# Performance work log

Hardware: AMD Instinct MI355X
Metric: run time of the kernel (lower is better)

## Reference

```python
import jax, jax.numpy as jnp
import numpy as np


def _interp_linear_align_corners(w, new_len):
    """Linear (bilinear with trivial 2nd axis) interpolation along last axis,
    align_corners=True, matching torch F.interpolate. w: (..., k) -> (..., new_len)."""
    k = w.shape[-1]
    scale = (k - 1) / (new_len - 1) if new_len > 1 else 0.0
    pos = jnp.arange(new_len, dtype=w.dtype) * jnp.asarray(scale, w.dtype)
    lo = jnp.floor(pos).astype(jnp.int32)
    hi = jnp.minimum(lo + 1, k - 1)
    frac = pos - lo.astype(w.dtype)
    return w[..., lo] * (1.0 - frac) + w[..., hi] * frac


def _depthwise_conv(x, kernel, pad_h, pad_w):
    # x: (B,C,H,W), kernel: (C,1,Kh,Kw), groups=C
    C = x.shape[1]
    return jax.lax.conv_general_dilated(
        x, kernel, window_strides=(1, 1),
        padding=[(pad_h, pad_h), (pad_w, pad_w)],
        dimension_numbers=("NCHW", "OIHW", "NCHW"),
        feature_group_count=C)


def setup_inputs() -> dict:
    key = jax.random.key(0)
    k1, k2, k3, k4, k5 = jax.random.split(key, 5)
    dim, ksize = 128, 13
    B, H, W = 32, 64, 64
    fan = 1.0 / np.sqrt(ksize)  # torch Conv2d default init scale (groups=dim -> fan_in=k)
    return {
        "x": jax.random.normal(k1, (B, dim, H, W), dtype=jnp.float32),
        "h_weight": jax.random.uniform(k2, (dim, 1, ksize, 1), jnp.float32, -fan, fan),
        "w_weight": jax.random.uniform(k3, (dim, 1, 1, ksize), jnp.float32, -fan, fan),
        "h_bias": jax.random.uniform(k4, (dim,), jnp.float32, -fan, fan),
        "w_bias": jax.random.uniform(k5, (dim,), jnp.float32, -fan, fan),
    }


def reference(x, h_weight, w_weight, h_bias, w_bias):
    B, C, H, W = x.shape
    Kh, Kw = 2 * H - 1, 2 * W - 1
    # Interpolate base kernels to instance kernel sizes (align_corners=True bilinear,
    # degenerate to 1-D linear since the other spatial dim has size 1).
    hk = _interp_linear_align_corners(h_weight[:, :, :, 0], Kh)[..., None]   # (C,1,Kh,1)
    wk = _interp_linear_align_corners(w_weight[:, :, 0, :], Kw)[:, :, None]  # (C,1,1,Kw)
    y = _depthwise_conv(x, hk, H - 1, 0) + h_bias[None, :, None, None]
    y = _depthwise_conv(y, wk, 0, W - 1) + w_bias[None, :, None, None]
    return y
```

## Files before the change

kernel.cpp:

```cpp
#include <hip/hip_runtime.h>


#define STRB 72

typedef short  bfrag  __attribute__((ext_vector_type(8)));
typedef float  f32x4  __attribute__((ext_vector_type(4)));
typedef unsigned short us4 __attribute__((ext_vector_type(4)));

__device__ __forceinline__ unsigned short f2bf(float f) {
    unsigned u = __builtin_bit_cast(unsigned, f);
    u += 0x7fffu + ((u >> 16) & 1u);
    return (unsigned short)(u >> 16);
}

__device__ __forceinline__ void lds_barrier() {
    asm volatile("s_waitcnt lgkmcnt(0)" ::: "memory");
    __builtin_amdgcn_s_barrier();
}

__global__ __launch_bounds__(256, 4)
void oversize_conv_mfma4(const float* __restrict__ x,
                         const float* __restrict__ hwt,
                         const float* __restrict__ wwt,
                         const float* __restrict__ hb,
                         const float* __restrict__ wb,
                         float* __restrict__ out)
{
    __shared__ __align__(16) unsigned short Xs[64 * STRB];
    __shared__ __align__(16) unsigned short Aw[64 * STRB];
    __shared__ __align__(16) unsigned short Ah[64 * STRB];
    __shared__ __align__(16) unsigned short PT[64 * STRB];
    __shared__ float hk[128], wk[128], sw[64];

    const int tid = threadIdx.x;
    const int c   = blockIdx.x & 127;
    const int g4  = blockIdx.x >> 7;
    const size_t img0      = ((size_t)(4 * g4) * 128 + c) * 4096;
    const size_t imgStride = (size_t)128 * 4096;

    const int wv = tid >> 6, lane = tid & 63;
    const int r = lane & 15, gq = lane >> 4;

    float4 xv[4];
    {
        const float4* xg = (const float4*)(x + img0);
        #pragma unroll
        for (int i = 0; i < 4; ++i) xv[i] = xg[tid + i * 256];
    }

    if (tid < 127) {
        const float scale = 12.0f / 126.0f;
        float pos = (float)tid * scale;
        int   lo  = (int)pos;
        float fr  = pos - (float)lo;
        int   hi  = (lo + 1 < 12) ? lo + 1 : 12;
        hk[tid] = hwt[c * 13 + lo] * (1.0f - fr) + hwt[c * 13 + hi] * fr;
        wk[tid] = wwt[c * 13 + lo] * (1.0f - fr) + wwt[c * 13 + hi] * fr;
    }
    lds_barrier();

    {
        const int row = tid >> 2;
        const int cb  = (tid & 3) * 16;
        #pragma unroll
        for (int q = 0; q < 4; ++q) {
            us4 vh, vw;
            #pragma unroll
            for (int j = 0; j < 4; ++j) {
                int col = cb + q * 4 + j;
                vh[j] = f2bf(hk[col - row + 63]);
                vw[j] = f2bf(wk[col - row + 63]);
            }
            *(us4*)&Ah[row * STRB + cb + q * 4] = vh;
            *(us4*)&Aw[row * STRB + cb + q * 4] = vw;
        }
    }
    if (tid < 64) {
        float s = 0.f;
        #pragma unroll 8
        for (int iw = 0; iw < 64; ++iw) s += wk[iw - tid + 63];
        sw[tid] = s;
    }
    #pragma unroll
    for (int i = 0; i < 4; ++i) {
        int idx = tid + i * 256;
        int row = idx >> 4;
        int col = (idx & 15) * 4;
        us4 v;
        v[0] = f2bf(xv[i].x); v[1] = f2bf(xv[i].y);
        v[2] = f2bf(xv[i].z); v[3] = f2bf(xv[i].w);
        *(us4*)&Xs[row * STRB + col] = v;
    }
    lds_barrier();

    const float hbc = hb[c], wbc = wb[c];
    float bias_nt[4];
    #pragma unroll
    for (int nt = 0; nt < 4; ++nt) bias_nt[nt] = hbc * sw[nt * 16 + r] + wbc;

    float4 xn[4];

    #pragma unroll
    for (int i = 0; i < 4; ++i) {
        if (i < 3) {
            const float4* xg = (const float4*)(x + img0 + (size_t)(i + 1) * imgStride);
            #pragma unroll
            for (int q = 0; q < 4; ++q) xn[q] = xg[tid + q * 256];
        }

        f32x4 acc[4] = {};
        {
            bfrag a0 = *(const bfrag*)&Xs[(wv * 16 + r) * STRB + gq * 8];
            bfrag a1 = *(const bfrag*)&Xs[(wv * 16 + r) * STRB + 32 + gq * 8];
            #pragma unroll
            for (int nt = 0; nt < 4; ++nt) {
                bfrag b0 = *(const bfrag*)&Aw[(nt * 16 + r) * STRB + gq * 8];
                bfrag b1 = *(const bfrag*)&Aw[(nt * 16 + r) * STRB + 32 + gq * 8];
                acc[nt] = __builtin_amdgcn_mfma_f32_16x16x32_bf16(a0, b0, acc[nt], 0, 0, 0);
                acc[nt] = __builtin_amdgcn_mfma_f32_16x16x32_bf16(a1, b1, acc[nt], 0, 0, 0);
            }
        }
        #pragma unroll
        for (int nt = 0; nt < 4; ++nt) {
            us4 p;
            p[0] = f2bf(acc[nt][0]); p[1] = f2bf(acc[nt][1]);
            p[2] = f2bf(acc[nt][2]); p[3] = f2bf(acc[nt][3]);
            *(us4*)&PT[(nt * 16 + r) * STRB + wv * 16 + gq * 4] = p;
        }
        lds_barrier();

        f32x4 acc2[4];
        #pragma unroll
        for (int nt = 0; nt < 4; ++nt) {
            float bv = bias_nt[nt];
            acc2[nt] = (f32x4){bv, bv, bv, bv};
        }
        {
            bfrag a0 = *(const bfrag*)&Ah[(wv * 16 + r) * STRB + gq * 8];
            bfrag a1 = *(const bfrag*)&Ah[(wv * 16 + r) * STRB + 32 + gq * 8];
            #pragma unroll
            for (int nt = 0; nt < 4; ++nt) {
                bfrag b0 = *(const bfrag*)&PT[(nt * 16 + r) * STRB + gq * 8];
                bfrag b1 = *(const bfrag*)&PT[(nt * 16 + r) * STRB + 32 + gq * 8];
                acc2[nt] = __builtin_amdgcn_mfma_f32_16x16x32_bf16(a0, b0, acc2[nt], 0, 0, 0);
                acc2[nt] = __builtin_amdgcn_mfma_f32_16x16x32_bf16(a1, b1, acc2[nt], 0, 0, 0);
            }
        }

        if (i < 3) {
            #pragma unroll
            for (int q = 0; q < 4; ++q) {
                int idx = tid + q * 256;
                int row = idx >> 4;
                int col = (idx & 15) * 4;
                us4 v;
                v[0] = f2bf(xn[q].x); v[1] = f2bf(xn[q].y);
                v[2] = f2bf(xn[q].z); v[3] = f2bf(xn[q].w);
                *(us4*)&Xs[row * STRB + col] = v;
            }
        }

        {
            float* og = out + img0 + (size_t)i * imgStride;
            #pragma unroll
            for (int nt = 0; nt < 4; ++nt) {
                #pragma unroll
                for (int j = 0; j < 4; ++j)
                    og[(size_t)(wv * 16 + gq * 4 + j) * 64 + nt * 16 + r] = acc2[nt][j];
            }
        }

        lds_barrier();
    }
}

extern "C" void kernel_launch(void* const* d_in, const int* in_sizes, int n_in,
                              void* d_out, int out_size, void* d_ws, size_t ws_size,
                              hipStream_t stream)
{
    const float* x   = (const float*)d_in[0];
    const float* hwt = (const float*)d_in[1];
    const float* wwt = (const float*)d_in[2];
    const float* hb  = (const float*)d_in[3];
    const float* wb  = (const float*)d_in[4];
    oversize_conv_mfma4<<<1024, 256, 0, stream>>>(x, hwt, wwt, hb, wb, (float*)d_out);
}
```

Before: 25.99 us.

## Load X fragments directly to registers, halve images per block, vectorize stores

X tiles are now read straight from global memory into MFMA A-fragments, so the Xs LDS staging buffer and its extra barrier pass go away. Each block now handles 2 images instead of 4, doubling the grid to 2048 blocks and raising launch bounds occupancy to 5. The second GEMM swaps operands so the PT tile is the A fragment and the output can be written as float4 stores along contiguous rows. The column-sum for the bias is split across all threads with a partial reduction. Smaller per-block work means the Toeplitz matrices are rebuilt more often, and the uncoalesced fragment-shaped global loads could cost bandwidth.

Measured after the change: 27.36 us. 1.05x slower.

```diff
diff --git a/kernel.cpp b/kernel.cpp
--- a/kernel.cpp
+++ b/kernel.cpp
@@ -18,35 +18,34 @@
     __builtin_amdgcn_s_barrier();
 }
 
-__global__ __launch_bounds__(256, 4)
-void oversize_conv_mfma4(const float* __restrict__ x,
+__global__ __launch_bounds__(256, 5)
+void oversize_conv_mfma2(const float* __restrict__ x,
                          const float* __restrict__ hwt,
                          const float* __restrict__ wwt,
                          const float* __restrict__ hb,
                          const float* __restrict__ wb,
                          float* __restrict__ out)
 {
-    __shared__ __align__(16) unsigned short Xs[64 * STRB];
     __shared__ __align__(16) unsigned short Aw[64 * STRB];
     __shared__ __align__(16) unsigned short Ah[64 * STRB];
     __shared__ __align__(16) unsigned short PT[64 * STRB];
-    __shared__ float hk[128], wk[128], sw[64];
+    __shared__ float hk[128], wk[128], swp[256];
+    __shared__ __align__(16) float sw[64];
 
     const int tid = threadIdx.x;
     const int c   = blockIdx.x & 127;
-    const int g4  = blockIdx.x >> 7;
-    const size_t img0      = ((size_t)(4 * g4) * 128 + c) * 4096;
+    const int bb  = (blockIdx.x >> 7) * 2;
+    const size_t img0      = ((size_t)bb * 128 + c) * 4096;
     const size_t imgStride = (size_t)128 * 4096;
 
     const int wv = tid >> 6, lane = tid & 63;
     const int r = lane & 15, gq = lane >> 4;
 
-    float4 xv[4];
-    {
-        const float4* xg = (const float4*)(x + img0);
-        #pragma unroll
-        for (int i = 0; i < 4; ++i) xv[i] = xg[tid + i * 256];
-    }
+    const float4* xrow0 = (const float4*)(x + img0 + (size_t)(16 * wv + r) * 64);
+    float4 xa0 = xrow0[2 * gq];
+    float4 xa1 = xrow0[2 * gq + 1];
+    float4 xa2 = xrow0[8 + 2 * gq];
+    float4 xa3 = xrow0[9 + 2 * gq];
 
     if (tid < 127) {
         const float scale = 12.0f / 126.0f;
@@ -75,50 +74,46 @@
             *(us4*)&Aw[row * STRB + cb + q * 4] = vw;
         }
     }
-    if (tid < 64) {
+    {
+        const int ow = tid >> 2, q = tid & 3;
         float s = 0.f;
-        #pragma unroll 8
-        for (int iw = 0; iw < 64; ++iw) s += wk[iw - tid + 63];
-        sw[tid] = s;
-    }
-    #pragma unroll
-    for (int i = 0; i < 4; ++i) {
-        int idx = tid + i * 256;
-        int row = idx >> 4;
-        int col = (idx & 15) * 4;
-        us4 v;
-        v[0] = f2bf(xv[i].x); v[1] = f2bf(xv[i].y);
-        v[2] = f2bf(xv[i].z); v[3] = f2bf(xv[i].w);
-        *(us4*)&Xs[row * STRB + col] = v;
+        #pragma unroll
+        for (int i = 0; i < 16; ++i) s += wk[(q * 16 + i) - ow + 63];
+        swp[tid] = s;
     }
     lds_barrier();
+    if (tid < 64)
+        sw[tid] = swp[4 * tid] + swp[4 * tid + 1] + swp[4 * tid + 2] + swp[4 * tid + 3];
 
     const float hbc = hb[c], wbc = wb[c];
-    float bias_nt[4];
-    #pragma unroll
-    for (int nt = 0; nt < 4; ++nt) bias_nt[nt] = hbc * sw[nt * 16 + r] + wbc;
-
-    float4 xn[4];
 
     #pragma unroll
-    for (int i = 0; i < 4; ++i) {
-        if (i < 3) {
-            const float4* xg = (const float4*)(x + img0 + (size_t)(i + 1) * imgStride);
-            #pragma unroll
-            for (int q = 0; q < 4; ++q) xn[q] = xg[tid + q * 256];
+    for (int i = 0; i < 2; ++i) {
+        bfrag a0, a1;
+        a0[0] = (short)f2bf(xa0.x); a0[1] = (short)f2bf(xa0.y);
+        a0[2] = (short)f2bf(xa0.z); a0[3] = (short)f2bf(xa0.w);
+        a0[4] = (short)f2bf(xa1.x); a0[5] = (short)f2bf(xa1.y);
+        a0[6] = (short)f2bf(xa1.z); a0[7] = (short)f2bf(xa1.w);
+        a1[0] = (short)f2bf(xa2.x); a1[1] = (short)f2bf(xa2.y);
+        a1[2] = (short)f2bf(xa2.z); a1[3] = (short)f2bf(xa2.w);
+        a1[4] = (short)f2bf(xa3.x); a1[5] = (short)f2bf(xa3.y);
+        a1[6] = (short)f2bf(xa3.z); a1[7] = (short)f2bf(xa3.w);
+
+        if (i == 0) {
+            const float4* xr = (const float4*)(x + img0 + imgStride + (size_t)(16 * wv + r) * 64);
+            xa0 = xr[2 * gq];
+            xa1 = xr[2 * gq + 1];
+            xa2 = xr[8 + 2 * gq];
+            xa3 = xr[9 + 2 * gq];
         }
 
         f32x4 acc[4] = {};
-        {
-            bfrag a0 = *(const bfrag*)&Xs[(wv * 16 + r) * STRB + gq * 8];
-            bfrag a1 = *(const bfrag*)&Xs[(wv * 16 + r) * STRB + 32 + gq * 8];
-            #pragma unroll
-            for (int nt = 0; nt < 4; ++nt) {
-                bfrag b0 = *(const bfrag*)&Aw[(nt * 16 + r) * STRB + gq * 8];
-                bfrag b1 = *(const bfrag*)&Aw[(nt * 16 + r) * STRB + 32 + gq * 8];
-                acc[nt] = __builtin_amdgcn_mfma_f32_16x16x32_bf16(a0, b0, acc[nt], 0, 0, 0);
-                acc[nt] = __builtin_amdgcn_mfma_f32_16x16x32_bf16(a1, b1, acc[nt], 0, 0, 0);
-            }
+        #pragma unroll
+        for (int nt = 0; nt < 4; ++nt) {
+            bfrag b0 = *(const bfrag*)&Aw[(nt * 16 + r) * STRB + gq * 8];
+            bfrag b1 = *(const bfrag*)&Aw[(nt * 16 + r) * STRB + 32 + gq * 8];
+            acc[nt] = __builtin_amdgcn_mfma_f32_16x16x32_bf16(a0, b0, acc[nt], 0, 0, 0);
+            acc[nt] = __builtin_amdgcn_mfma_f32_16x16x32_bf16(a1, b1, acc[nt], 0, 0, 0);
         }
         #pragma unroll
         for (int nt = 0; nt < 4; ++nt) {
@@ -129,45 +124,29 @@
         }
         lds_barrier();
 
-        f32x4 acc2[4];
+        f32x4 sw4 = *(const f32x4*)&sw[16 * wv + 4 * gq];
+        f32x4 bias;
+        bias[0] = hbc * sw4[0] + wbc; bias[1] = hbc * sw4[1] + wbc;
+        bias[2] = hbc * sw4[2] + wbc; bias[3] = hbc * sw4[3] + wbc;
+
+        bfrag pa0 = *(const bfrag*)&PT[(16 * wv + r) * STRB + gq * 8];
+        bfrag pa1 = *(const bfrag*)&PT[(16 * wv + r) * STRB + 32 + gq * 8];
+        f32x4 acc2[4] = {bias, bias, bias, bias};
         #pragma unroll
         for (int nt = 0; nt < 4; ++nt) {
-            float bv = bias_nt[nt];
-            acc2[nt] = (f32x4){bv, bv, bv, bv};
-        }
-        {
-            bfrag a0 = *(const bfrag*)&Ah[(wv * 16 + r) * STRB + gq * 8];
-            bfrag a1 = *(const bfrag*)&Ah[(wv * 16 + r) * STRB + 32 + gq * 8];
-            #pragma unroll
-            for (int nt = 0; nt < 4; ++nt) {
-                bfrag b0 = *(const bfrag*)&PT[(nt * 16 + r) * STRB + gq * 8];
-                bfrag b1 = *(const bfrag*)&PT[(nt * 16 + r) * STRB + 32 + gq * 8];
-                acc2[nt] = __builtin_amdgcn_mfma_f32_16x16x32_bf16(a0, b0, acc2[nt], 0, 0, 0);
-                acc2[nt] = __builtin_amdgcn_mfma_f32_16x16x32_bf16(a1, b1, acc2[nt], 0, 0, 0);
-            }
+            bfrag bh0 = *(const bfrag*)&Ah[(nt * 16 + r) * STRB + gq * 8];
+            bfrag bh1 = *(const bfrag*)&Ah[(nt * 16 + r) * STRB + 32 + gq * 8];
+            acc2[nt] = __builtin_amdgcn_mfma_f32_16x16x32_bf16(pa0, bh0, acc2[nt], 0, 0, 0);
+            acc2[nt] = __builtin_amdgcn_mfma_f32_16x16x32_bf16(pa1, bh1, acc2[nt], 0, 0, 0);
         }
 
-        if (i < 3) {
-            #pragma unroll
-            for (int q = 0; q < 4; ++q) {
-                int idx = tid + q * 256;
-                int row = idx >> 4;
-                int col = (idx & 15) * 4;
-                us4 v;
-                v[0] = f2bf(xn[q].x); v[1] = f2bf(xn[q].y);
-                v[2] = f2bf(xn[q].z); v[3] = f2bf(xn[q].w);
-                *(us4*)&Xs[row * STRB + col] = v;
-            }
-        }
-
-        {
-            float* og = out + img0 + (size_t)i * imgStride;
-            #pragma unroll
-            for (int nt = 0; nt < 4; ++nt) {
-                #pragma unroll
-                for (int j = 0; j < 4; ++j)
-                    og[(size_t)(wv * 16 + gq * 4 + j) * 64 + nt * 16 + r] = acc2[nt][j];
-            }
+        float* og = out + img0 + (size_t)i * imgStride;
+        #pragma unroll
+        for (int nt = 0; nt < 4; ++nt) {
+            float4 v;
+            v.x = acc2[nt][0]; v.y = acc2[nt][1];
+            v.z = acc2[nt][2]; v.w = acc2[nt][3];
+            *(float4*)&og[(size_t)(nt * 16 + r) * 64 + 16 * wv + 4 * gq] = v;
         }
 
         lds_barrier();
@@ -183,5 +162,5 @@
     const float* wwt = (const float*)d_in[2];
     const float* hb  = (const float*)d_in[3];
     const float* wb  = (const float*)d_in[4];
-    oversize_conv_mfma4<<<1024, 256, 0, stream>>>(x, hwt, wwt, hb, wb, (float*)d_out);
+    oversize_conv_mfma2<<<2048, 256, 0, stream>>>(x, hwt, wwt, hb, wb, (float*)d_out);
 }
```

## Swap second GEMM operands for vectorized nontemporal stores and earlier prefetch

Applied to the files above, without the earlier changes.

The second MFMA stage now takes the intermediate tile PT as the A operand and the height kernel as B. The output fragment becomes row-contiguous, so each lane writes a float4 with a nontemporal store instead of four strided scalar stores. The next image's global load is issued before the first barrier and overlapped with the following iteration's compute. The bias row-sum reduction is also split across all 256 threads instead of 64. The intended gain is wider, fully coalesced output writes and more latency hiding, in exchange for a changed bias layout and higher register pressure from the longer-lived prefetch.

Measured after the change: 30.43 us. 17.1% more time.

```diff
diff --git a/kernel.cpp b/kernel.cpp
--- a/kernel.cpp
+++ b/kernel.cpp
@@ -19,24 +19,25 @@
 }
 
 __global__ __launch_bounds__(256, 4)
-void oversize_conv_mfma4(const float* __restrict__ x,
-                         const float* __restrict__ hwt,
-                         const float* __restrict__ wwt,
-                         const float* __restrict__ hb,
-                         const float* __restrict__ wb,
-                         float* __restrict__ out)
+void oversize_conv_v5(const float* __restrict__ x,
+                      const float* __restrict__ hwt,
+                      const float* __restrict__ wwt,
+                      const float* __restrict__ hb,
+                      const float* __restrict__ wb,
+                      float* __restrict__ out)
 {
     __shared__ __align__(16) unsigned short Xs[64 * STRB];
     __shared__ __align__(16) unsigned short Aw[64 * STRB];
     __shared__ __align__(16) unsigned short Ah[64 * STRB];
     __shared__ __align__(16) unsigned short PT[64 * STRB];
-    __shared__ float hk[128], wk[128], sw[64];
+    __shared__ float hk[128], wk[128], swp[256];
+    __shared__ __align__(16) float sw[64];
 
     const int tid = threadIdx.x;
     const int c   = blockIdx.x & 127;
     const int g4  = blockIdx.x >> 7;
-    const size_t img0      = ((size_t)(4 * g4) * 128 + c) * 4096;
     const size_t imgStride = (size_t)128 * 4096;
+    const size_t img0 = ((size_t)(4 * g4) * 128 + c) * 4096;
 
     const int wv = tid >> 6, lane = tid & 63;
     const int r = lane & 15, gq = lane >> 4;
@@ -45,7 +46,7 @@
     {
         const float4* xg = (const float4*)(x + img0);
         #pragma unroll
-        for (int i = 0; i < 4; ++i) xv[i] = xg[tid + i * 256];
+        for (int q = 0; q < 4; ++q) xv[q] = xg[tid + q * 256];
     }
 
     if (tid < 127) {
@@ -75,76 +76,71 @@
             *(us4*)&Aw[row * STRB + cb + q * 4] = vw;
         }
     }
-    if (tid < 64) {
+    {
+        const int ow = tid >> 2, q = tid & 3;
         float s = 0.f;
-        #pragma unroll 8
-        for (int iw = 0; iw < 64; ++iw) s += wk[iw - tid + 63];
-        sw[tid] = s;
+        #pragma unroll
+        for (int i = 0; i < 16; ++i) s += wk[(q * 16 + i) - ow + 63];
+        swp[tid] = s;
     }
     #pragma unroll
-    for (int i = 0; i < 4; ++i) {
-        int idx = tid + i * 256;
+    for (int q = 0; q < 4; ++q) {
+        int idx = tid + q * 256;
         int row = idx >> 4;
         int col = (idx & 15) * 4;
         us4 v;
-        v[0] = f2bf(xv[i].x); v[1] = f2bf(xv[i].y);
-        v[2] = f2bf(xv[i].z); v[3] = f2bf(xv[i].w);
+        v[0] = f2bf(xv[q].x); v[1] = f2bf(xv[q].y);
+        v[2] = f2bf(xv[q].z); v[3] = f2bf(xv[q].w);
         *(us4*)&Xs[row * STRB + col] = v;
+    }
+    float4 xn[4];
+    {
+        const float4* xg = (const float4*)(x + img0 + imgStride);
+        #pragma unroll
+        for (int q = 0; q < 4; ++q) xn[q] = xg[tid + q * 256];
     }
     lds_barrier();
 
+    if (tid < 64)
+        sw[tid] = swp[4 * tid] + swp[4 * tid + 1] + swp[4 * tid + 2] + swp[4 * tid + 3];
+
     const float hbc = hb[c], wbc = wb[c];
-    float bias_nt[4];
-    #pragma unroll
-    for (int nt = 0; nt < 4; ++nt) bias_nt[nt] = hbc * sw[nt * 16 + r] + wbc;
-
-    float4 xn[4];
 
     #pragma unroll
     for (int i = 0; i < 4; ++i) {
-        if (i < 3) {
-            const float4* xg = (const float4*)(x + img0 + (size_t)(i + 1) * imgStride);
-            #pragma unroll
-            for (int q = 0; q < 4; ++q) xn[q] = xg[tid + q * 256];
-        }
-
+        bfrag a0 = *(const bfrag*)&Xs[(16 * wv + r) * STRB + 8 * gq];
+        bfrag a1 = *(const bfrag*)&Xs[(16 * wv + r) * STRB + 32 + 8 * gq];
         f32x4 acc[4] = {};
-        {
-            bfrag a0 = *(const bfrag*)&Xs[(wv * 16 + r) * STRB + gq * 8];
-            bfrag a1 = *(const bfrag*)&Xs[(wv * 16 + r) * STRB + 32 + gq * 8];
-            #pragma unroll
-            for (int nt = 0; nt < 4; ++nt) {
-                bfrag b0 = *(const bfrag*)&Aw[(nt * 16 + r) * STRB + gq * 8];
-                bfrag b1 = *(const bfrag*)&Aw[(nt * 16 + r) * STRB + 32 + gq * 8];
-                acc[nt] = __builtin_amdgcn_mfma_f32_16x16x32_bf16(a0, b0, acc[nt], 0, 0, 0);
-                acc[nt] = __builtin_amdgcn_mfma_f32_16x16x32_bf16(a1, b1, acc[nt], 0, 0, 0);
-            }
+        #pragma unroll
+        for (int nt = 0; nt < 4; ++nt) {
+            bfrag b0 = *(const bfrag*)&Aw[(16 * nt + r) * STRB + 8 * gq];
+            bfrag b1 = *(const bfrag*)&Aw[(16 * nt + r) * STRB + 32 + 8 * gq];
+            acc[nt] = __builtin_amdgcn_mfma_f32_16x16x32_bf16(a0, b0, acc[nt], 0, 0, 0);
+            acc[nt] = __builtin_amdgcn_mfma_f32_16x16x32_bf16(a1, b1, acc[nt], 0, 0, 0);
         }
         #pragma unroll
         for (int nt = 0; nt < 4; ++nt) {
             us4 p;
             p[0] = f2bf(acc[nt][0]); p[1] = f2bf(acc[nt][1]);
             p[2] = f2bf(acc[nt][2]); p[3] = f2bf(acc[nt][3]);
-            *(us4*)&PT[(nt * 16 + r) * STRB + wv * 16 + gq * 4] = p;
+            *(us4*)&PT[(16 * nt + r) * STRB + 16 * wv + 4 * gq] = p;
         }
         lds_barrier();
 
-        f32x4 acc2[4];
+        f32x4 sw4 = *(const f32x4*)&sw[16 * wv + 4 * gq];
+        f32x4 bias;
+        bias[0] = hbc * sw4[0] + wbc; bias[1] = hbc * sw4[1] + wbc;
+        bias[2] = hbc * sw4[2] + wbc; bias[3] = hbc * sw4[3] + wbc;
+
+        bfrag pa0 = *(const bfrag*)&PT[(16 * wv + r) * STRB + 8 * gq];
+        bfrag pa1 = *(const bfrag*)&PT[(16 * wv + r) * STRB + 32 + 8 * gq];
+        f32x4 acc2[4] = {bias, bias, bias, bias};
         #pragma unroll
         for (int nt = 0; nt < 4; ++nt) {
-            float bv = bias_nt[nt];
-            acc2[nt] = (f32x4){bv, bv, bv, bv};
-        }
-        {
-            bfrag a0 = *(const bfrag*)&Ah[(wv * 16 + r) * STRB + gq * 8];
-            bfrag a1 = *(const bfrag*)&Ah[(wv * 16 + r) * STRB + 32 + gq * 8];
-            #pragma unroll
-            for (int nt = 0; nt < 4; ++nt) {
-                bfrag b0 = *(const bfrag*)&PT[(nt * 16 + r) * STRB + gq * 8];
-                bfrag b1 = *(const bfrag*)&PT[(nt * 16 + r) * STRB + 32 + gq * 8];
-                acc2[nt] = __builtin_amdgcn_mfma_f32_16x16x32_bf16(a0, b0, acc2[nt], 0, 0, 0);
-                acc2[nt] = __builtin_amdgcn_mfma_f32_16x16x32_bf16(a1, b1, acc2[nt], 0, 0, 0);
-            }
+            bfrag bh0 = *(const bfrag*)&Ah[(16 * nt + r) * STRB + 8 * gq];
+            bfrag bh1 = *(const bfrag*)&Ah[(16 * nt + r) * STRB + 32 + 8 * gq];
+            acc2[nt] = __builtin_amdgcn_mfma_f32_16x16x32_bf16(pa0, bh0, acc2[nt], 0, 0, 0);
+            acc2[nt] = __builtin_amdgcn_mfma_f32_16x16x32_bf16(pa1, bh1, acc2[nt], 0, 0, 0);
         }
 
         if (i < 3) {
@@ -159,14 +155,19 @@
                 *(us4*)&Xs[row * STRB + col] = v;
             }
         }
+        if (i < 2) {
+            const float4* xg = (const float4*)(x + img0 + (size_t)(i + 2) * imgStride);
+            #pragma unroll
+            for (int q = 0; q < 4; ++q) xn[q] = xg[tid + q * 256];
+        }
 
         {
             float* og = out + img0 + (size_t)i * imgStride;
             #pragma unroll
             for (int nt = 0; nt < 4; ++nt) {
-                #pragma unroll
-                for (int j = 0; j < 4; ++j)
-                    og[(size_t)(wv * 16 + gq * 4 + j) * 64 + nt * 16 + r] = acc2[nt][j];
+                __builtin_nontemporal_store(
+                    acc2[nt],
+                    (f32x4*)&og[(size_t)(16 * nt + r) * 64 + 16 * wv + 4 * gq]);
             }
         }
 
@@ -183,5 +184,5 @@
     const float* wwt = (const float*)d_in[2];
     const float* hb  = (const float*)d_in[3];
     const float* wb  = (const float*)d_in[4];
-    oversize_conv_mfma4<<<1024, 256, 0, stream>>>(x, hwt, wwt, hb, wb, (float*)d_out);
+    oversize_conv_v5<<<1024, 256, 0, stream>>>(x, hwt, wwt, hb, wb, (float*)d_out);
 }
```
